# Optimization experiments

Hardware: AMD Instinct MI355X
Metric: run time of the kernel (lower is better)

## Reference

```python
import jax, jax.numpy as jnp
from jax import lax
import numpy as np
import math

EPS = 1e-5
NBINS = 17   # quantized color levels round(x*255/16) for x in [0,1)
K_MODE = 11

def _bn(x, g, b):
    # BatchNorm2d in training mode: batch statistics over (B,H,W)
    m = jnp.mean(x, axis=(0, 2, 3), keepdims=True)
    v = jnp.var(x, axis=(0, 2, 3), keepdims=True)
    return (x - m) * lax.rsqrt(v + EPS) * g[None, :, None, None] + b[None, :, None, None]

def _lrelu(x):
    return jnp.where(x >= 0, x, 0.01 * x)

def _shared_conv(x, w, b, stride, padding):
    # one KxK kernel shared depthwise across all channels, scalar bias
    C = x.shape[1]
    k = jnp.tile(w[None, None], (C, 1, 1, 1))  # (C,1,K,K)
    y = lax.conv_general_dilated(x, k, (stride, stride),
                                 [(padding, padding), (padding, padding)],
                                 dimension_numbers=('NCHW', 'OIHW', 'NCHW'),
                                 feature_group_count=C)
    return y + b[0]

def _avg_pool_same(x, k):
    # avg_pool2d(k, stride=1, padding=k//2, count_include_pad=True)
    p = k // 2
    s = lax.reduce_window(x, 0.0, lax.add, (1, 1, k, k), (1, 1, 1, 1),
                          [(0, 0), (0, 0), (p, p), (p, p)])
    return s / float(k * k)

def _mode_pool(xq):
    # xq values are exact multiples of 16/256 -> recover integer bin index,
    # then mode over 11x11 window = argmax of per-bin counts (histogram).
    # torch zero-padding corresponds to bin 0; argmax first-max tie-break ->
    # smallest value, matching torch.mode.
    q = jnp.clip(jnp.round(xq * (256.0 / 16.0)).astype(jnp.int32), 0, NBINS - 1)
    pad = K_MODE // 2
    qp = jnp.pad(q, ((0, 0), (0, 0), (pad, pad), (pad, pad)))
    onehot = (qp[:, :, None] == jnp.arange(NBINS, dtype=jnp.int32)[None, None, :, None, None]).astype(jnp.float32)
    counts = lax.reduce_window(onehot, 0.0, lax.add, (1, 1, 1, K_MODE, K_MODE), (1, 1, 1, 1, 1), 'VALID')
    mode_bin = jnp.argmax(counts, axis=2)  # (B,C,H,W)
    return mode_bin.astype(xq.dtype) * (16.0 / 256.0)

def _forward(x, p_w1, p_b1, p_dw1, p_db1, p_g1, p_be1,
             p_w2, p_b2, p_dw2, p_db2, p_g2, p_be2,
             d_w, d_b, ia_w, ia_b, ia_g, ia_be,
             ib_w, ib_b, ib_g, ib_be,
             f_g1, f_be1, f_g2, f_be2):
    xq = jnp.round(x * (255.0 / 16.0)) * (16.0 / 256.0)
    xm = _mode_pool(xq)
    B, C, H, W = xm.shape
    half = p_w1.shape[0]

    # prepare: 1x1 conv -> depthwise 1x1 (per-channel scale) -> BN -> LeakyReLU, twice
    h = jnp.einsum('bchw,oc->bohw', xm, p_w1) + p_b1[None, :, None, None]
    h = h * p_dw1[None, :, None, None] + p_db1[None, :, None, None]
    h = _lrelu(_bn(h, p_g1, p_be1))
    h = jnp.einsum('bchw,oc->bohw', h, p_w2) + p_b2[None, :, None, None]
    h = h * p_dw2[None, :, None, None] + p_db2[None, :, None, None]
    h = _lrelu(_bn(h, p_g2, p_be2))

    n = int(math.floor(math.log(min(H, W), 3)))
    score = jnp.zeros((B, 2 * half, H, W), x.dtype)
    d = h
    for _ in range(n):
        d = _shared_conv(d, d_w, d_b, 3, 1)  # stride-3 downgrade
        z = jax.image.resize(d, (B, half, H, W), method='bilinear')
        a = _lrelu(_bn(_shared_conv(z, ia_w, ia_b, 1, 2), ia_g, ia_be))
        bb = _lrelu(_bn(_shared_conv(z, ib_w, ib_b, 1, 2), ib_g, ib_be))
        score = score + jnp.concatenate([a, bb], axis=1)  # Splitter + Stack(1)

    def ft(s):
        s = _bn(s, f_g1, f_be1)
        s = jnp.where(s > 0.1, 0.1 + 0.7 * (s - 0.1), s)  # MaxLeakyReLU(0.7, 0.1)
        s = _bn(s, f_g2, f_be2)
        return 2.0 * s - _avg_pool_same(s, K_MODE)  # EmphaseLocal(11): x + (x - local mean)

    score = ft(ft(ft(score)))
    return score / n

def setup_inputs() -> dict:
    key = jax.random.key(0)
    ks = jax.random.split(key, 32)
    B, Cin, H, W, half = 8, 3, 384, 384, 32
    r = lambda i, shp, s=0.1: s * jax.random.normal(ks[i], shp, dtype=jnp.float32)
    g = lambda i, shp: 1.0 + 0.1 * jax.random.normal(ks[i], shp, dtype=jnp.float32)
    return dict(
        x=jax.random.uniform(ks[0], (B, Cin, H, W), dtype=jnp.float32),
        p_w1=r(1, (half, Cin), 0.3), p_b1=r(2, (half,)),
        p_dw1=g(3, (half,)), p_db1=r(4, (half,)),
        p_g1=g(5, (half,)), p_be1=r(6, (half,)),
        p_w2=r(7, (half, half), 0.2), p_b2=r(8, (half,)),
        p_dw2=g(9, (half,)), p_db2=r(10, (half,)),
        p_g2=g(11, (half,)), p_be2=r(12, (half,)),
        d_w=r(13, (3, 3), 0.2), d_b=r(14, (1,)),
        ia_w=r(15, (5, 5), 0.2), ia_b=r(16, (1,)),
        ia_g=g(17, (half,)), ia_be=r(18, (half,)),
        ib_w=r(19, (5, 5), 0.2), ib_b=r(20, (1,)),
        ib_g=g(21, (half,)), ib_be=r(22, (half,)),
        f_g1=g(23, (2 * half,)), f_be1=r(24, (2 * half,)),
        f_g2=g(25, (2 * half,)), f_be2=r(26, (2 * half,)),
    )

def reference(x, p_w1, p_b1, p_dw1, p_db1, p_g1, p_be1,
              p_w2, p_b2, p_dw2, p_db2, p_g2, p_be2,
              d_w, d_b, ia_w, ia_b, ia_g, ia_be,
              ib_w, ib_b, ib_g, ib_be,
              f_g1, f_be1, f_g2, f_be2):
    return _forward(x, p_w1, p_b1, p_dw1, p_db1, p_g1, p_be1,
                    p_w2, p_b2, p_dw2, p_db2, p_g2, p_be2,
                    d_w, d_b, ia_w, ia_b, ia_g, ia_be,
                    ib_w, ib_b, ib_g, ib_be,
                    f_g1, f_be1, f_g2, f_be2)
```

## Files before the change

kernel.cpp:

```cpp
#include <hip/hip_runtime.h>

#define HW 147456
#define WID 384
#define NB 8
#define NPC 1179648
#define HW4 36864

static __device__ __forceinline__ float lrelu01(float v) { return v >= 0.f ? v : 0.01f * v; }
static __device__ __forceinline__ float mlrelu(float v) { return v > 0.1f ? 0.1f + 0.7f * (v - 0.1f) : v; }

__global__ __launch_bounds__(256) void mode_kernel(const float* __restrict__ x,
                                                   float* __restrict__ xm) {
  __shared__ unsigned char qt[26 * 76];
  __shared__ unsigned int cc[16 * 5 * 76];
  const int plane = blockIdx.z;
  const int x0 = blockIdx.x * 64;
  const int y0 = blockIdx.y * 16;
  const float* xp = x + (size_t)plane * HW;

  for (int i = threadIdx.x; i < 26 * 76; i += 256) {
    int r = i / 76, ccol = i - r * 76;
    int gy = y0 + r - 5, gx = x0 + ccol - 5;
    unsigned char q = 0;
    if (ccol < 74 && gy >= 0 && gy < WID && gx >= 0 && gx < WID) {
      float v = xp[gy * WID + gx];
      int qi = (int)rintf(v * 15.9375f);
      qi = qi < 0 ? 0 : (qi > 16 ? 16 : qi);
      q = (unsigned char)qi;
    }
    qt[i] = q;
  }
  __syncthreads();

  for (int i = threadIdx.x; i < 16 * 74; i += 256) {
    int yy = i / 74, col = i - yy * 74;
    unsigned int w0 = 0, w1 = 0, w2 = 0, w3 = 0, w4 = 0;
#pragma unroll
    for (int dy = 0; dy < 11; ++dy) {
      int q = qt[(yy + dy) * 76 + col];
      unsigned int inc = 1u << ((q & 3) << 3);
      int wsel = q >> 2;
      w0 += (wsel == 0) ? inc : 0u;
      w1 += (wsel == 1) ? inc : 0u;
      w2 += (wsel == 2) ? inc : 0u;
      w3 += (wsel == 3) ? inc : 0u;
      w4 += (wsel == 4) ? inc : 0u;
    }
    cc[(yy * 5 + 0) * 76 + col] = w0;
    cc[(yy * 5 + 1) * 76 + col] = w1;
    cc[(yy * 5 + 2) * 76 + col] = w2;
    cc[(yy * 5 + 3) * 76 + col] = w3;
    cc[(yy * 5 + 4) * 76 + col] = w4;
  }
  __syncthreads();

  for (int i = threadIdx.x; i < 16 * 64; i += 256) {
    int yy = i / 64, xx = i - yy * 64;
    unsigned int s0 = 0, s1 = 0, s2 = 0, s3 = 0, s4 = 0;
#pragma unroll
    for (int dx = 0; dx < 11; ++dx) {
      int col = xx + dx;
      s0 += cc[(yy * 5 + 0) * 76 + col];
      s1 += cc[(yy * 5 + 1) * 76 + col];
      s2 += cc[(yy * 5 + 2) * 76 + col];
      s3 += cc[(yy * 5 + 3) * 76 + col];
      s4 += cc[(yy * 5 + 4) * 76 + col];
    }
    unsigned int words[5] = {s0, s1, s2, s3, s4};
    int best = 0;
    unsigned int bc = s0 & 0xffu;
#pragma unroll
    for (int bin = 1; bin < 17; ++bin) {
      unsigned int cnt = (words[bin >> 2] >> ((bin & 3) * 8)) & 0xffu;
      if (cnt > bc) { bc = cnt; best = bin; }
    }
    xm[(size_t)plane * HW + (size_t)(y0 + yy) * WID + (x0 + xx)] = best * 0.0625f;
  }
}

__global__ __launch_bounds__(256) void xm_mom(const float4* __restrict__ X,
                                              float* __restrict__ part9) {
  float s0 = 0, s1 = 0, s2 = 0, m00 = 0, m01 = 0, m02 = 0, m11 = 0, m12 = 0, m22 = 0;
  const int end = (blockIdx.x + 1) * 1152;
  for (int u = blockIdx.x * 1152 + threadIdx.x; u < end; u += 256) {
    int b = u / HW4, p4 = u - b * HW4;
    const float4* base = X + (size_t)b * 3 * HW4 + p4;
    float4 a = base[0], bb = base[HW4], c = base[2 * HW4];
    s0 += a.x + a.y + a.z + a.w;
    s1 += bb.x + bb.y + bb.z + bb.w;
    s2 += c.x + c.y + c.z + c.w;
    m00 += a.x * a.x + a.y * a.y + a.z * a.z + a.w * a.w;
    m01 += a.x * bb.x + a.y * bb.y + a.z * bb.z + a.w * bb.w;
    m02 += a.x * c.x + a.y * c.y + a.z * c.z + a.w * c.w;
    m11 += bb.x * bb.x + bb.y * bb.y + bb.z * bb.z + bb.w * bb.w;
    m12 += bb.x * c.x + bb.y * c.y + bb.z * c.z + bb.w * c.w;
    m22 += c.x * c.x + c.y * c.y + c.z * c.z + c.w * c.w;
  }
  float vals[9] = {s0, s1, s2, m00, m01, m02, m11, m12, m22};
  int lane = threadIdx.x & 63, wd = threadIdx.x >> 6;
  __shared__ float red[4][9];
#pragma unroll
  for (int j = 0; j < 9; ++j) {
    float v = vals[j];
    for (int off = 32; off; off >>= 1) v += __shfl_down(v, off);
    if (lane == 0) red[wd][j] = v;
  }
  __syncthreads();
  if (threadIdx.x < 9)
    part9[blockIdx.x * 9 + threadIdx.x] =
        red[0][threadIdx.x] + red[1][threadIdx.x] + red[2][threadIdx.x] + red[3][threadIdx.x];
}

__global__ __launch_bounds__(64) void prep1_affine(const float* __restrict__ part9,
                                                   const float* __restrict__ w1,
                                                   const float* __restrict__ b1,
                                                   const float* __restrict__ dw1,
                                                   const float* __restrict__ db1,
                                                   const float* __restrict__ g,
                                                   const float* __restrict__ be,
                                                   float* __restrict__ sc,
                                                   float* __restrict__ sh) {
  __shared__ double M[9];
  if (threadIdx.x < 9) {
    double s = 0.0;
    for (int i = 0; i < 256; ++i) s += (double)part9[i * 9 + threadIdx.x];
    M[threadIdx.x] = s;
  }
  __syncthreads();
  if (threadIdx.x < 32) {
    int o = threadIdx.x;
    double dw = dw1[o];
    double a0 = (double)w1[o * 3] * dw, a1 = (double)w1[o * 3 + 1] * dw,
           a2 = (double)w1[o * 3 + 2] * dw;
    double k = (double)b1[o] * dw + (double)db1[o];
    double N = (double)NPC;
    double lin = (a0 * M[0] + a1 * M[1] + a2 * M[2]) / N;
    double mean = lin + k;
    double e2 = (a0 * a0 * M[3] + a1 * a1 * M[6] + a2 * a2 * M[8] +
                 2.0 * (a0 * a1 * M[4] + a0 * a2 * M[5] + a1 * a2 * M[7])) / N +
                2.0 * k * lin + k * k;
    double var = e2 - mean * mean;
    float rstd = rsqrtf((float)var + 1e-5f);
    float scl = rstd * g[o];
    sc[o] = scl;
    sh[o] = be[o] - (float)mean * scl;
  }
}

__global__ __launch_bounds__(256) void prep_fused(const float* __restrict__ xm,
                                                  const float* __restrict__ w1,
                                                  const float* __restrict__ b1,
                                                  const float* __restrict__ dw1,
                                                  const float* __restrict__ db1,
                                                  const float* __restrict__ P1SC,
                                                  const float* __restrict__ P1SH,
                                                  const float* __restrict__ w2,
                                                  const float* __restrict__ b2,
                                                  const float* __restrict__ dw2,
                                                  const float* __restrict__ db2,
                                                  float* __restrict__ t2,
                                                  float* __restrict__ part) {
  __shared__ float wl[1024];
  __shared__ float c1[32][4];
  __shared__ float bias2[32];
  __shared__ float wred[8][32];
  for (int i = threadIdx.x; i < 1024; i += 256) wl[i] = w2[i] * dw2[i >> 5];
  if (threadIdx.x < 32) {
    int o = threadIdx.x;
    float dw = dw1[o], s1 = P1SC[o];
    c1[o][0] = w1[o * 3] * dw * s1;
    c1[o][1] = w1[o * 3 + 1] * dw * s1;
    c1[o][2] = w1[o * 3 + 2] * dw * s1;
    c1[o][3] = (b1[o] * dw + db1[o]) * s1 + P1SH[o];
    bias2[o] = b2[o] * dw2[o] + db2[o];
  }
  __syncthreads();
  const int p0 = blockIdx.x * 512 + threadIdx.x;
  const int b = p0 / HW, pp = p0 - b * HW;
  const float* xb = xm + (size_t)b * 3 * HW + pp;
  float h[2][32];
#pragma unroll
  for (int q = 0; q < 2; ++q) {
    float x0 = xb[q * 256], x1 = xb[HW + q * 256], x2 = xb[2 * HW + q * 256];
#pragma unroll
    for (int o = 0; o < 32; ++o) {
      float u = fmaf(x0, c1[o][0], fmaf(x1, c1[o][1], fmaf(x2, c1[o][2], c1[o][3])));
      h[q][o] = lrelu01(u);
    }
  }
  float sv[32], sq[32];
  float* ob = t2 + (size_t)b * 32 * HW + pp;
  const float4* wl4 = reinterpret_cast<const float4*>(wl);
  for (int o = 0; o < 32; ++o) {
    float acc0 = bias2[o], acc1 = bias2[o];
#pragma unroll
    for (int c4 = 0; c4 < 8; ++c4) {
      float4 w4 = wl4[o * 8 + c4];
      int c = c4 * 4;
      acc0 = fmaf(h[0][c], w4.x, acc0);     acc1 = fmaf(h[1][c], w4.x, acc1);
      acc0 = fmaf(h[0][c + 1], w4.y, acc0); acc1 = fmaf(h[1][c + 1], w4.y, acc1);
      acc0 = fmaf(h[0][c + 2], w4.z, acc0); acc1 = fmaf(h[1][c + 2], w4.z, acc1);
      acc0 = fmaf(h[0][c + 3], w4.w, acc0); acc1 = fmaf(h[1][c + 3], w4.w, acc1);
    }
    ob[(size_t)o * HW] = acc0;
    ob[(size_t)o * HW + 256] = acc1;
    sv[o] = acc0 + acc1;
    sq[o] = acc0 * acc0 + acc1 * acc1;
  }
  int lane = threadIdx.x & 63, wd = threadIdx.x >> 6;
#pragma unroll
  for (int o = 0; o < 32; ++o) {
    float a = sv[o], q = sq[o];
    for (int off = 32; off; off >>= 1) {
      a += __shfl_down(a, off);
      q += __shfl_down(q, off);
    }
    if (lane == 0) { wred[wd][o] = a; wred[wd + 4][o] = q; }
  }
  __syncthreads();
  if (threadIdx.x < 32) {
    int o = threadIdx.x;
    part[((size_t)o * 2304 + blockIdx.x) * 2] = wred[0][o] + wred[1][o] + wred[2][o] + wred[3][o];
    part[((size_t)o * 2304 + blockIdx.x) * 2 + 1] = wred[4][o] + wred[5][o] + wred[6][o] + wred[7][o];
  }
}

__global__ __launch_bounds__(64) void stats_combine(const float* __restrict__ part, int nsplit,
                                                    const float* __restrict__ g,
                                                    const float* __restrict__ be,
                                                    float* __restrict__ sc,
                                                    float* __restrict__ sh) {
  const int c = blockIdx.x;
  double s = 0.0, q = 0.0;
  for (int i = threadIdx.x; i < nsplit; i += 64) {
    s += part[((size_t)c * nsplit + i) * 2];
    q += part[((size_t)c * nsplit + i) * 2 + 1];
  }
  for (int off = 32; off; off >>= 1) {
    s += __shfl_down(s, off);
    q += __shfl_down(q, off);
  }
  if (threadIdx.x == 0) {
    double mean = s / (double)NPC;
    double var = q / (double)NPC - mean * mean;
    float rstd = rsqrtf((float)var + 1e-5f);
    float scl = rstd * g[c];
    sc[c] = scl;
    sh[c] = be[c] - (float)mean * scl;
  }
}

template <bool AFF>
__global__ __launch_bounds__(256) void dconv(const float* __restrict__ in,
                                             const float* __restrict__ sc,
                                             const float* __restrict__ sh,
                                             const float* __restrict__ w9,
                                             const float* __restrict__ db,
                                             int Sin, int Sout,
                                             float* __restrict__ out, int total) {
  int idx = blockIdx.x * 256 + threadIdx.x;
  if (idx >= total) return;
  int xx = idx % Sout;
  int t = idx / Sout;
  int yy = t % Sout;
  int pc = t / Sout;
  int c = pc & 31;
  const float* ip = in + (size_t)pc * Sin * Sin;
  float a = AFF ? sc[c] : 1.f;
  float h = AFF ? sh[c] : 0.f;
  float acc = 0.f;
#pragma unroll
  for (int ky = 0; ky < 3; ++ky) {
    int iy = 3 * yy - 1 + ky;
    if (iy < 0 || iy >= Sin) continue;
#pragma unroll
    for (int kx = 0; kx < 3; ++kx) {
      int ix = 3 * xx - 1 + kx;
      if (ix < 0 || ix >= Sin) continue;
      float v = ip[(size_t)iy * Sin + ix];
      if (AFF) { v = v * a + h; v = lrelu01(v); }
      acc = fmaf(v, w9[ky * 3 + kx], acc);
    }
  }
  out[idx] = acc + db[0];
}

static __device__ __forceinline__ int sin_of(int l) {
  return l == 0 ? 128 : l == 1 ? 43 : l == 2 ? 15 : l == 3 ? 5 : 2;
}

__device__ __forceinline__ void conv_ab(const float* zt, int row, int g,
                                        const float* wa, const float* wb,
                                        float ba0, float bb0, float* A, float* Bv) {
  float aa0 = ba0, aa1 = ba0, aa2 = ba0, aa3 = ba0;
  float eb0 = bb0, eb1 = bb0, eb2 = bb0, eb3 = bb0;
#pragma unroll
  for (int dy = 0; dy < 5; ++dy) {
    const float* zr = &zt[(row + dy) * 40 + g * 4];
    float4 zlo = *reinterpret_cast<const float4*>(zr);
    float4 zhi = *reinterpret_cast<const float4*>(zr + 4);
    float z[8] = {zlo.x, zlo.y, zlo.z, zlo.w, zhi.x, zhi.y, zhi.z, zhi.w};
#pragma unroll
    for (int dx = 0; dx < 5; ++dx) {
      float wva = wa[dy * 5 + dx], wvb = wb[dy * 5 + dx];
      aa0 = fmaf(z[dx], wva, aa0);
      aa1 = fmaf(z[dx + 1], wva, aa1);
      aa2 = fmaf(z[dx + 2], wva, aa2);
      aa3 = fmaf(z[dx + 3], wva, aa3);
      eb0 = fmaf(z[dx], wvb, eb0);
      eb1 = fmaf(z[dx + 1], wvb, eb1);
      eb2 = fmaf(z[dx + 2], wvb, eb2);
      eb3 = fmaf(z[dx + 3], wvb, eb3);
    }
  }
  A[0] = aa0; A[1] = aa1; A[2] = aa2; A[3] = aa3;
  Bv[0] = eb0; Bv[1] = eb1; Bv[2] = eb2; Bv[3] = eb3;
}

__global__ __launch_bounds__(256) void upstats2(const float* __restrict__ d1,
                                                const float* __restrict__ d2,
                                                const float* __restrict__ d3,
                                                const float* __restrict__ d4,
                                                const float* __restrict__ d5,
                                                const float* __restrict__ wA5,
                                                const float* __restrict__ wB5,
                                                const float* __restrict__ bA,
                                                const float* __restrict__ bB,
                                                float* __restrict__ partA,
                                                float* __restrict__ partB) {
  __shared__ __align__(16) float zt[2][36 * 40];
  __shared__ __align__(16) float dH[2][16 * 40];
  __shared__ int gx0[36], gx1[36], gy0[36], gy1[36];
  __shared__ float gfx[36], gfy[36], gxv[36], gyv[36];
  __shared__ float red[2][16];
  const int lvl = blockIdx.z;
  const float* dsel = lvl == 0 ? d1 : lvl == 1 ? d2 : lvl == 2 ? d3 : lvl == 3 ? d4 : d5;
  const int Sin = sin_of(lvl);
  const float scale = (float)Sin / 384.f;
  const int plane0 = blockIdx.y * 2, tile = blockIdx.x;
  const int tx = (tile % 12) * 32, ty = (tile / 12) * 32;

  if (threadIdx.x < 72) {
    int t = threadIdx.x >= 36 ? threadIdx.x - 36 : threadIdx.x;
    bool isY = threadIdx.x >= 36;
    int gp = (isY ? ty : tx) + t - 2;
    float valid = (gp >= 0 && gp < WID) ? 1.f : 0.f;
    int gpc = gp < 0 ? 0 : (gp >= WID ? WID - 1 : gp);
    float s = (gpc + 0.5f) * scale - 0.5f;
    float f0 = floorf(s);
    float fr = s - f0;
    int ii = (int)f0;
    int i1 = ii + 1 < Sin - 1 ? ii + 1 : Sin - 1;
    int i0 = ii > 0 ? ii : 0;
    if (isY) { gy0[t] = i0; gy1[t] = i1; gfy[t] = fr; gyv[t] = valid; }
    else     { gx0[t] = i0; gx1[t] = i1; gfx[t] = fr; gxv[t] = valid; }
  }
  float wa[25], wb[25];
#pragma unroll
  for (int k = 0; k < 25; ++k) { wa[k] = wA5[k]; wb[k] = wB5[k]; }
  const float ba0 = bA[0], bb0 = bB[0];
  __syncthreads();

  const int rowlo = gy0[0], nrows = gy1[35] - rowlo + 1;
  const int cnt = nrows * 36;
  for (int i = threadIdx.x; i < 2 * cnt; i += 256) {
    int p = i < cnt ? 0 : 1;
    int j = i - p * cnt;
    int r = j / 36, zx = j - r * 36;
    const float* drow = dsel + (size_t)(plane0 + p) * Sin * Sin + (size_t)(rowlo + r) * Sin;
    float v0 = drow[gx0[zx]], v1 = drow[gx1[zx]];
    dH[p][r * 40 + zx] = (v0 + gfx[zx] * (v1 - v0)) * gxv[zx];
  }
  __syncthreads();
  for (int i = threadIdx.x; i < 648; i += 256) {
    int p = i < 324 ? 0 : 1;
    int j = i - p * 324;
    int zy = j / 9, k = j - zy * 9;
    int r0 = gy0[zy] - rowlo, r1 = gy1[zy] - rowlo;
    float fy = gfy[zy], vv = gyv[zy];
    float4 a4 = *reinterpret_cast<const float4*>(&dH[p][r0 * 40 + k * 4]);
    float4 b4 = *reinterpret_cast<const float4*>(&dH[p][r1 * 40 + k * 4]);
    float4 o;
    o.x = (a4.x + fy * (b4.x - a4.x)) * vv;
    o.y = (a4.y + fy * (b4.y - a4.y)) * vv;
    o.z = (a4.z + fy * (b4.z - a4.z)) * vv;
    o.w = (a4.w + fy * (b4.w - a4.w)) * vv;
    *reinterpret_cast<float4*>(&zt[p][zy * 40 + k * 4]) = o;
  }
  __syncthreads();

  const int row = threadIdx.x >> 3, g = threadIdx.x & 7;
  const int lane = threadIdx.x & 63, wd = threadIdx.x >> 6;
#pragma unroll
  for (int p = 0; p < 2; ++p) {
    float A[4], Bv[4];
    conv_ab(zt[p], row, g, wa, wb, ba0, bb0, A, Bv);
    float sa = A[0] + A[1] + A[2] + A[3];
    float qa = A[0] * A[0] + A[1] * A[1] + A[2] * A[2] + A[3] * A[3];
    float sb = Bv[0] + Bv[1] + Bv[2] + Bv[3];
    float qb = Bv[0] * Bv[0] + Bv[1] * Bv[1] + Bv[2] * Bv[2] + Bv[3] * Bv[3];
    for (int off = 32; off; off >>= 1) {
      sa += __shfl_down(sa, off); qa += __shfl_down(qa, off);
      sb += __shfl_down(sb, off); qb += __shfl_down(qb, off);
    }
    if (lane == 0) {
      red[p][wd * 4 + 0] = sa; red[p][wd * 4 + 1] = qa;
      red[p][wd * 4 + 2] = sb; red[p][wd * 4 + 3] = qb;
    }
  }
  __syncthreads();
  if (threadIdx.x < 2) {
    int p = threadIdx.x;
    int plane = plane0 + p;
    int b = plane >> 5, c = plane & 31;
    const float* r_ = red[p];
    size_t pi = (size_t)lvl * 73728 + ((size_t)c * 1152 + (size_t)b * 144 + tile) * 2;
    partA[pi] = r_[0] + r_[4] + r_[8] + r_[12];
    partA[pi + 1] = r_[1] + r_[5] + r_[9] + r_[13];
    partB[pi] = r_[2] + r_[6] + r_[10] + r_[14];
    partB[pi + 1] = r_[3] + r_[7] + r_[11] + r_[15];
  }
}

__global__ __launch_bounds__(64) void combine_lvls(const float* __restrict__ partA,
                                                   const float* __restrict__ partB,
                                                   const float* __restrict__ ia_g,
                                                   const float* __restrict__ ia_be,
                                                   const float* __restrict__ ib_g,
                                                   const float* __restrict__ ib_be,
                                                   float* __restrict__ aff) {
  const int c = blockIdx.x, lvl = blockIdx.y, z = blockIdx.z;
  const float* part = (z ? partB : partA) + (size_t)lvl * 73728;
  const float* g = z ? ib_g : ia_g;
  const float* be = z ? ib_be : ia_be;
  double s = 0.0, q = 0.0;
  for (int i = threadIdx.x; i < 1152; i += 64) {
    s += part[((size_t)c * 1152 + i) * 2];
    q += part[((size_t)c * 1152 + i) * 2 + 1];
  }
  for (int off = 32; off; off >>= 1) {
    s += __shfl_down(s, off);
    q += __shfl_down(q, off);
  }
  if (threadIdx.x == 0) {
    double mean = s / (double)NPC;
    double var = q / (double)NPC - mean * mean;
    float rstd = rsqrtf((float)var + 1e-5f);
    float scl = rstd * g[c];
    aff[((z * 5 + lvl) * 2 + 0) * 32 + c] = scl;
    aff[((z * 5 + lvl) * 2 + 1) * 32 + c] = be[c] - (float)mean * scl;
  }
}

__global__ __launch_bounds__(256) void apply_all(const float* __restrict__ d1,
                                                 const float* __restrict__ d2,
                                                 const float* __restrict__ d3,
                                                 const float* __restrict__ d4,
                                                 const float* __restrict__ d5,
                                                 const float* __restrict__ wA5,
                                                 const float* __restrict__ wB5,
                                                 const float* __restrict__ bA,
                                                 const float* __restrict__ bB,
                                                 const float* __restrict__ aff,
                                                 float* __restrict__ outp,
                                                 float* __restrict__ partF) {
  __shared__ __align__(16) float zt[36 * 40];
  __shared__ __align__(16) float dH[16 * 40];
  __shared__ int gx0[5][36], gx1[5][36], gy0[5][36], gy1[5][36];
  __shared__ float gfx[5][36], gfy[5][36], gxv[5][36], gyv[5][36];
  __shared__ float red[16];
  const int plane = blockIdx.y, tile = blockIdx.x;
  const int tx = (tile % 12) * 32, ty = (tile / 12) * 32;
  const int b = plane >> 5, c = plane & 31;
  float wa[25], wb[25];
#pragma unroll
  for (int k = 0; k < 25; ++k) { wa[k] = wA5[k]; wb[k] = wB5[k]; }
  const float ba0 = bA[0], bb0 = bB[0];
  const int row = threadIdx.x >> 3, g = threadIdx.x & 7;

  for (int i = threadIdx.x; i < 360; i += 256) {
    int l = i / 72, j = i - l * 72;
    int t = j >= 36 ? j - 36 : j;
    bool isY = j >= 36;
    int Sin = sin_of(l);
    float scale = (float)Sin / 384.f;
    int gp = (isY ? ty : tx) + t - 2;
    float valid = (gp >= 0 && gp < WID) ? 1.f : 0.f;
    int gpc = gp < 0 ? 0 : (gp >= WID ? WID - 1 : gp);
    float s = (gpc + 0.5f) * scale - 0.5f;
    float f0 = floorf(s);
    float fr = s - f0;
    int ii = (int)f0;
    int i1 = ii + 1 < Sin - 1 ? ii + 1 : Sin - 1;
    int i0 = ii > 0 ? ii : 0;
    if (isY) { gy0[l][t] = i0; gy1[l][t] = i1; gfy[l][t] = fr; gyv[l][t] = valid; }
    else     { gx0[l][t] = i0; gx1[l][t] = i1; gfx[l][t] = fr; gxv[l][t] = valid; }
  }
  __syncthreads();

  float acA[4] = {0.f, 0.f, 0.f, 0.f}, acB[4] = {0.f, 0.f, 0.f, 0.f};
  for (int l = 0; l < 5; ++l) {
    const float* dsel = l == 0 ? d1 : l == 1 ? d2 : l == 2 ? d3 : l == 3 ? d4 : d5;
    const int Sin = sin_of(l);
    const float* dp = dsel + (size_t)plane * Sin * Sin;
    const int rowlo = gy0[l][0], nrows = gy1[l][35] - rowlo + 1;
    for (int i = threadIdx.x; i < nrows * 36; i += 256) {
      int r = i / 36, zx = i - r * 36;
      const float* drow = dp + (size_t)(rowlo + r) * Sin;
      float v0 = drow[gx0[l][zx]], v1 = drow[gx1[l][zx]];
      dH[r * 40 + zx] = (v0 + gfx[l][zx] * (v1 - v0)) * gxv[l][zx];
    }
    __syncthreads();
    for (int i = threadIdx.x; i < 324; i += 256) {
      int zy = i / 9, k = i - zy * 9;
      int r0 = gy0[l][zy] - rowlo, r1 = gy1[l][zy] - rowlo;
      float fy = gfy[l][zy], vv = gyv[l][zy];
      float4 a4 = *reinterpret_cast<const float4*>(&dH[r0 * 40 + k * 4]);
      float4 b4 = *reinterpret_cast<const float4*>(&dH[r1 * 40 + k * 4]);
      float4 o;
      o.x = (a4.x + fy * (b4.x - a4.x)) * vv;
      o.y = (a4.y + fy * (b4.y - a4.y)) * vv;
      o.z = (a4.z + fy * (b4.z - a4.z)) * vv;
      o.w = (a4.w + fy * (b4.w - a4.w)) * vv;
      *reinterpret_cast<float4*>(&zt[zy * 40 + k * 4]) = o;
    }
    __syncthreads();
    float A[4], Bv[4];
    conv_ab(zt, row, g, wa, wb, ba0, bb0, A, Bv);
    float as = aff[(l * 2 + 0) * 32 + c], ah = aff[(l * 2 + 1) * 32 + c];
    float bs = aff[((5 + l) * 2 + 0) * 32 + c], bh = aff[((5 + l) * 2 + 1) * 32 + c];
#pragma unroll
    for (int j = 0; j < 4; ++j) {
      acA[j] += lrelu01(fmaf(A[j], as, ah));
      acB[j] += lrelu01(fmaf(Bv[j], bs, bh));
    }
  }
  float4 xa = {acA[0], acA[1], acA[2], acA[3]};
  float4 xb = {acB[0], acB[1], acB[2], acB[3]};
  size_t po = (size_t)(b * 64 + c) * HW + (size_t)(ty + row) * WID + tx + g * 4;
  *reinterpret_cast<float4*>(outp + po) = xa;
  *reinterpret_cast<float4*>(outp + po + (size_t)32 * HW) = xb;

  float sa = xa.x + xa.y + xa.z + xa.w;
  float qa = xa.x * xa.x + xa.y * xa.y + xa.z * xa.z + xa.w * xa.w;
  float sb = xb.x + xb.y + xb.z + xb.w;
  float qb = xb.x * xb.x + xb.y * xb.y + xb.z * xb.z + xb.w * xb.w;
  int lane = threadIdx.x & 63, wd = threadIdx.x >> 6;
  for (int off = 32; off; off >>= 1) {
    sa += __shfl_down(sa, off); qa += __shfl_down(qa, off);
    sb += __shfl_down(sb, off); qb += __shfl_down(qb, off);
  }
  __syncthreads();
  if (lane == 0) {
    red[wd * 4 + 0] = sa; red[wd * 4 + 1] = qa;
    red[wd * 4 + 2] = sb; red[wd * 4 + 3] = qb;
  }
  __syncthreads();
  if (threadIdx.x == 0) {
    size_t piA = ((size_t)c * 1152 + (size_t)b * 144 + tile) * 2;
    size_t piB = ((size_t)(c + 32) * 1152 + (size_t)b * 144 + tile) * 2;
    partF[piA] = red[0] + red[4] + red[8] + red[12];
    partF[piA + 1] = red[1] + red[5] + red[9] + red[13];
    partF[piB] = red[2] + red[6] + red[10] + red[14];
    partF[piB + 1] = red[3] + red[7] + red[11] + red[15];
  }
}

__global__ __launch_bounds__(256) void stats_mlrelu(const float4* __restrict__ X,
                                                    const float* __restrict__ sc1,
                                                    const float* __restrict__ sh1,
                                                    float* __restrict__ part) {
  int c = blockIdx.x >> 6, s = blockIdx.x & 63;
  float a1 = sc1[c], b1 = sh1[c];
  float sum = 0.f, sq = 0.f;
  int b = s >> 3;
  const float4* Xp = X + (size_t)(b * 64 + c) * HW4 + (s & 7) * 4608 + threadIdx.x;
#pragma unroll 6
  for (int it = 0; it < 18; ++it) {
    float4 v = Xp[it * 256];
    float u;
    u = mlrelu(fmaf(v.x, a1, b1)); sum += u; sq += u * u;
    u = mlrelu(fmaf(v.y, a1, b1)); sum += u; sq += u * u;
    u = mlrelu(fmaf(v.z, a1, b1)); sum += u; sq += u * u;
    u = mlrelu(fmaf(v.w, a1, b1)); sum += u; sq += u * u;
  }
  int lane = threadIdx.x & 63, wd = threadIdx.x >> 6;
  for (int off = 32; off; off >>= 1) {
    sum += __shfl_down(sum, off);
    sq += __shfl_down(sq, off);
  }
  __shared__ float red[8];
  if (lane == 0) { red[wd * 2] = sum; red[wd * 2 + 1] = sq; }
  __syncthreads();
  if (threadIdx.x == 0) {
    part[((size_t)c * 64 + s) * 2] = red[0] + red[2] + red[4] + red[6];
    part[((size_t)c * 64 + s) * 2 + 1] = red[1] + red[3] + red[5] + red[7];
  }
}

__global__ __launch_bounds__(256) void ft_fused(const float* __restrict__ src,
                                                const float* __restrict__ F1SC,
                                                const float* __restrict__ F1SH,
                                                const float* __restrict__ F2SC,
                                                const float* __restrict__ F2SH,
                                                float* __restrict__ dst, float fscale,
                                                float* __restrict__ part) {
  __shared__ float sl[74 * 81];
  __shared__ __align__(16) float Hl[74 * 64];
  __shared__ float red[8];
  const int tile = blockIdx.x;
  const int plane = blockIdx.y;
  const int b = plane >> 6, c = plane & 63;
  const int tx = (tile % 6) * 64, ty = (tile / 6) * 64;
  const float a1 = F1SC[c], b1 = F1SH[c], a2 = F2SC[c], b2 = F2SH[c];
  const float* sp = src + (size_t)plane * HW;

  for (int i = threadIdx.x; i < 74 * 20; i += 256) {
    int r = i / 20, k = i - r * 20;
    int gy = ty + r - 5, gx = tx + k * 4 - 8;
    float4 sv = {0.f, 0.f, 0.f, 0.f};
    if (gy >= 0 && gy < WID && gx >= 0 && gx < WID) {
      float4 v = *reinterpret_cast<const float4*>(sp + (size_t)gy * WID + gx);
      sv.x = fmaf(mlrelu(fmaf(v.x, a1, b1)), a2, b2);
      sv.y = fmaf(mlrelu(fmaf(v.y, a1, b1)), a2, b2);
      sv.z = fmaf(mlrelu(fmaf(v.z, a1, b1)), a2, b2);
      sv.w = fmaf(mlrelu(fmaf(v.w, a1, b1)), a2, b2);
    }
    int base = r * 81 + k * 4;
    sl[base] = sv.x; sl[base + 1] = sv.y; sl[base + 2] = sv.z; sl[base + 3] = sv.w;
  }
  __syncthreads();

  for (int i = threadIdx.x; i < 74 * 16; i += 256) {
    int r = i >> 4, g = i & 15;
    const float* s0 = &sl[r * 81 + g * 4 + 3];
    float v[14];
#pragma unroll
    for (int j = 0; j < 14; ++j) v[j] = s0[j];
    float h0 = v[0] + v[1] + v[2] + v[3] + v[4] + v[5] + v[6] + v[7] + v[8] + v[9] + v[10];
    float h1 = h0 - v[0] + v[11];
    float h2 = h1 - v[1] + v[12];
    float h3 = h2 - v[2] + v[13];
    float4 hh = {h0, h1, h2, h3};
    *reinterpret_cast<float4*>(&Hl[r * 64 + g * 4]) = hh;
  }
  __syncthreads();

  const int g = threadIdx.x & 15, ly = threadIdx.x >> 4;
  const int y0 = ly * 4;
  const float4* H4 = reinterpret_cast<const float4*>(Hl);
  float4 acc = H4[y0 * 16 + g];
#pragma unroll
  for (int dy = 1; dy < 11; ++dy) {
    float4 t = H4[(y0 + dy) * 16 + g];
    acc.x += t.x; acc.y += t.y; acc.z += t.z; acc.w += t.w;
  }
  float sum = 0.f, sq = 0.f;
  float* dpo = dst + (size_t)plane * HW;
#pragma unroll
  for (int ry = 0; ry < 4; ++ry) {
    int y = y0 + ry;
    if (ry) {
      float4 ta = H4[(y + 10) * 16 + g];
      float4 tb = H4[(y - 1) * 16 + g];
      acc.x += ta.x - tb.x; acc.y += ta.y - tb.y;
      acc.z += ta.z - tb.z; acc.w += ta.w - tb.w;
    }
    const float* cp = &sl[(y + 5) * 81 + g * 4 + 8];
    float4 o;
    o.x = (2.f * cp[0] - acc.x * (1.f / 121.f)) * fscale;
    o.y = (2.f * cp[1] - acc.y * (1.f / 121.f)) * fscale;
    o.z = (2.f * cp[2] - acc.z * (1.f / 121.f)) * fscale;
    o.w = (2.f * cp[3] - acc.w * (1.f / 121.f)) * fscale;
    *reinterpret_cast<float4*>(dpo + (size_t)(ty + y) * WID + tx + g * 4) = o;
    sum += o.x + o.y + o.z + o.w;
    sq += o.x * o.x + o.y * o.y + o.z * o.z + o.w * o.w;
  }
  if (part) {
    int lane = threadIdx.x & 63, wd = threadIdx.x >> 6;
    for (int off = 32; off; off >>= 1) {
      sum += __shfl_down(sum, off);
      sq += __shfl_down(sq, off);
    }
    if (lane == 0) { red[wd * 2] = sum; red[wd * 2 + 1] = sq; }
    __syncthreads();
    if (threadIdx.x == 0) {
      size_t pi = ((size_t)c * 288 + (size_t)b * 36 + tile) * 2;
      part[pi] = red[0] + red[2] + red[4] + red[6];
      part[pi + 1] = red[1] + red[3] + red[5] + red[7];
    }
  }
}

extern "C" void kernel_launch(void* const* d_in, const int* in_sizes, int n_in,
                              void* d_out, int out_size, void* d_ws, size_t ws_size,
                              hipStream_t stream) {
  const float* x     = (const float*)d_in[0];
  const float* p_w1  = (const float*)d_in[1];
  const float* p_b1  = (const float*)d_in[2];
  const float* p_dw1 = (const float*)d_in[3];
  const float* p_db1 = (const float*)d_in[4];
  const float* p_g1  = (const float*)d_in[5];
  const float* p_be1 = (const float*)d_in[6];
  const float* p_w2  = (const float*)d_in[7];
  const float* p_b2  = (const float*)d_in[8];
  const float* p_dw2 = (const float*)d_in[9];
  const float* p_db2 = (const float*)d_in[10];
  const float* p_g2  = (const float*)d_in[11];
  const float* p_be2 = (const float*)d_in[12];
  const float* d_w   = (const float*)d_in[13];
  const float* d_b   = (const float*)d_in[14];
  const float* ia_w  = (const float*)d_in[15];
  const float* ia_b  = (const float*)d_in[16];
  const float* ia_g  = (const float*)d_in[17];
  const float* ia_be = (const float*)d_in[18];
  const float* ib_w  = (const float*)d_in[19];
  const float* ib_b  = (const float*)d_in[20];
  const float* ib_g  = (const float*)d_in[21];
  const float* ib_be = (const float*)d_in[22];
  const float* f_g1  = (const float*)d_in[23];
  const float* f_be1 = (const float*)d_in[24];
  const float* f_g2  = (const float*)d_in[25];
  const float* f_be2 = (const float*)d_in[26];
  float* out = (float*)d_out;
  float* ws = (float*)d_ws;

  const size_t SLOT = 37748736ull;
  float* B0 = ws;
  float* B1 = ws + 2 * SLOT;
  float* t2 = B0;
  float* partA = B0 + SLOT;
  float* partB = partA + 368640;
  float* partP = partB + 368640;
  float* part9 = partP + 147456;
  float* aff   = part9 + 2304;
  float* xm  = B1;
  float* dd1 = xm + 3538944;
  float* dd2 = dd1 + 4194304;
  float* dd3 = dd2 + 473344;
  float* dd4 = dd3 + 57600;
  float* dd5 = dd4 + 6400;
  float* partF = ws + 4 * SLOT;
  float* partS = partF + 147456;
  float* st    = partS + 8192;

  float* P1SC = st,       *P1SH = st + 32;
  float* P2SC = st + 64,  *P2SH = st + 96;
  float* F1SC = st + 128, *F1SH = st + 192;
  float* F2SC = st + 256, *F2SH = st + 320;

  mode_kernel<<<dim3(6, 24, 24), 256, 0, stream>>>(x, xm);
  xm_mom<<<256, 256, 0, stream>>>((const float4*)xm, part9);
  prep1_affine<<<1, 64, 0, stream>>>(part9, p_w1, p_b1, p_dw1, p_db1, p_g1, p_be1, P1SC, P1SH);
  prep_fused<<<2304, 256, 0, stream>>>(xm, p_w1, p_b1, p_dw1, p_db1, P1SC, P1SH,
                                       p_w2, p_b2, p_dw2, p_db2, t2, partP);
  stats_combine<<<32, 64, 0, stream>>>(partP, 2304, p_g2, p_be2, P2SC, P2SH);

  dconv<true><<<16384, 256, 0, stream>>>(t2, P2SC, P2SH, d_w, d_b, 384, 128, dd1,
                                         8 * 32 * 128 * 128);
  dconv<false><<<(8 * 32 * 43 * 43 + 255) / 256, 256, 0, stream>>>(
      dd1, nullptr, nullptr, d_w, d_b, 128, 43, dd2, 8 * 32 * 43 * 43);
  dconv<false><<<(8 * 32 * 15 * 15 + 255) / 256, 256, 0, stream>>>(
      dd2, nullptr, nullptr, d_w, d_b, 43, 15, dd3, 8 * 32 * 15 * 15);
  dconv<false><<<(8 * 32 * 5 * 5 + 255) / 256, 256, 0, stream>>>(
      dd3, nullptr, nullptr, d_w, d_b, 15, 5, dd4, 8 * 32 * 5 * 5);
  dconv<false><<<(8 * 32 * 2 * 2 + 255) / 256, 256, 0, stream>>>(
      dd4, nullptr, nullptr, d_w, d_b, 5, 2, dd5, 8 * 32 * 2 * 2);

  upstats2<<<dim3(144, 128, 5), 256, 0, stream>>>(dd1, dd2, dd3, dd4, dd5,
                                                  ia_w, ib_w, ia_b, ib_b, partA, partB);
  combine_lvls<<<dim3(32, 5, 2), 64, 0, stream>>>(partA, partB, ia_g, ia_be, ib_g, ib_be, aff);
  apply_all<<<dim3(144, 256), 256, 0, stream>>>(dd1, dd2, dd3, dd4, dd5,
                                                ia_w, ib_w, ia_b, ib_b, aff, out, partF);

  const float* cur = out;
  float* dsts[3] = {B0, B1, out};
  for (int k = 0; k < 3; ++k) {
    stats_combine<<<64, 64, 0, stream>>>(partF, (k == 0) ? 1152 : 288, f_g1, f_be1, F1SC, F1SH);
    stats_mlrelu<<<64 * 64, 256, 0, stream>>>((const float4*)cur, F1SC, F1SH, partS);
    stats_combine<<<64, 64, 0, stream>>>(partS, 64, f_g2, f_be2, F2SC, F2SH);
    ft_fused<<<dim3(36, 512), 256, 0, stream>>>(cur, F1SC, F1SH, F2SC, F2SH, dsts[k],
                                                (k == 2) ? 0.2f : 1.0f,
                                                (k < 2) ? partF : nullptr);
    cur = dsts[k];
  }
}
```

Baseline: 2.097 ms.

## Split pyramid upsample-conv into per-wave row strips with wave-local LDS fences

Measured after the change: 2.260 ms. +7.8%, slower.

```diff
diff --git a/kernel.cpp b/kernel.cpp
--- a/kernel.cpp
+++ b/kernel.cpp
@@ -8,6 +8,9 @@
 
 static __device__ __forceinline__ float lrelu01(float v) { return v >= 0.f ? v : 0.01f * v; }
 static __device__ __forceinline__ float mlrelu(float v) { return v > 0.1f ? 0.1f + 0.7f * (v - 0.1f) : v; }
+
+#define WFENCE() do { asm volatile("s_waitcnt lgkmcnt(0)" ::: "memory"); \
+                      __builtin_amdgcn_sched_barrier(0); } while (0)
 
 __global__ __launch_bounds__(256) void mode_kernel(const float* __restrict__ x,
                                                    float* __restrict__ xm) {
@@ -317,166 +320,36 @@
   Bv[0] = eb0; Bv[1] = eb1; Bv[2] = eb2; Bv[3] = eb3;
 }
 
-__global__ __launch_bounds__(256) void upstats2(const float* __restrict__ d1,
-                                                const float* __restrict__ d2,
-                                                const float* __restrict__ d3,
-                                                const float* __restrict__ d4,
-                                                const float* __restrict__ d5,
-                                                const float* __restrict__ wA5,
-                                                const float* __restrict__ wB5,
-                                                const float* __restrict__ bA,
-                                                const float* __restrict__ bB,
-                                                float* __restrict__ partA,
-                                                float* __restrict__ partB) {
-  __shared__ __align__(16) float zt[2][36 * 40];
-  __shared__ __align__(16) float dH[2][16 * 40];
-  __shared__ int gx0[36], gx1[36], gy0[36], gy1[36];
-  __shared__ float gfx[36], gfy[36], gxv[36], gyv[36];
-  __shared__ float red[2][16];
-  const int lvl = blockIdx.z;
-  const float* dsel = lvl == 0 ? d1 : lvl == 1 ? d2 : lvl == 2 ? d3 : lvl == 3 ? d4 : d5;
-  const int Sin = sin_of(lvl);
-  const float scale = (float)Sin / 384.f;
-  const int plane0 = blockIdx.y * 2, tile = blockIdx.x;
-  const int tx = (tile % 12) * 32, ty = (tile / 12) * 32;
-
-  if (threadIdx.x < 72) {
-    int t = threadIdx.x >= 36 ? threadIdx.x - 36 : threadIdx.x;
-    bool isY = threadIdx.x >= 36;
-    int gp = (isY ? ty : tx) + t - 2;
-    float valid = (gp >= 0 && gp < WID) ? 1.f : 0.f;
-    int gpc = gp < 0 ? 0 : (gp >= WID ? WID - 1 : gp);
-    float s = (gpc + 0.5f) * scale - 0.5f;
-    float f0 = floorf(s);
-    float fr = s - f0;
-    int ii = (int)f0;
-    int i1 = ii + 1 < Sin - 1 ? ii + 1 : Sin - 1;
-    int i0 = ii > 0 ? ii : 0;
-    if (isY) { gy0[t] = i0; gy1[t] = i1; gfy[t] = fr; gyv[t] = valid; }
-    else     { gx0[t] = i0; gx1[t] = i1; gfx[t] = fr; gxv[t] = valid; }
-  }
-  float wa[25], wb[25];
-#pragma unroll
-  for (int k = 0; k < 25; ++k) { wa[k] = wA5[k]; wb[k] = wB5[k]; }
-  const float ba0 = bA[0], bb0 = bB[0];
-  __syncthreads();
-
-  const int rowlo = gy0[0], nrows = gy1[35] - rowlo + 1;
-  const int cnt = nrows * 36;
-  for (int i = threadIdx.x; i < 2 * cnt; i += 256) {
-    int p = i < cnt ? 0 : 1;
-    int j = i - p * cnt;
-    int r = j / 36, zx = j - r * 36;
-    const float* drow = dsel + (size_t)(plane0 + p) * Sin * Sin + (size_t)(rowlo + r) * Sin;
-    float v0 = drow[gx0[zx]], v1 = drow[gx1[zx]];
-    dH[p][r * 40 + zx] = (v0 + gfx[zx] * (v1 - v0)) * gxv[zx];
-  }
-  __syncthreads();
-  for (int i = threadIdx.x; i < 648; i += 256) {
-    int p = i < 324 ? 0 : 1;
-    int j = i - p * 324;
-    int zy = j / 9, k = j - zy * 9;
-    int r0 = gy0[zy] - rowlo, r1 = gy1[zy] - rowlo;
-    float fy = gfy[zy], vv = gyv[zy];
-    float4 a4 = *reinterpret_cast<const float4*>(&dH[p][r0 * 40 + k * 4]);
-    float4 b4 = *reinterpret_cast<const float4*>(&dH[p][r1 * 40 + k * 4]);
-    float4 o;
-    o.x = (a4.x + fy * (b4.x - a4.x)) * vv;
-    o.y = (a4.y + fy * (b4.y - a4.y)) * vv;
-    o.z = (a4.z + fy * (b4.z - a4.z)) * vv;
-    o.w = (a4.w + fy * (b4.w - a4.w)) * vv;
-    *reinterpret_cast<float4*>(&zt[p][zy * 40 + k * 4]) = o;
-  }
-  __syncthreads();
-
-  const int row = threadIdx.x >> 3, g = threadIdx.x & 7;
-  const int lane = threadIdx.x & 63, wd = threadIdx.x >> 6;
-#pragma unroll
-  for (int p = 0; p < 2; ++p) {
-    float A[4], Bv[4];
-    conv_ab(zt[p], row, g, wa, wb, ba0, bb0, A, Bv);
-    float sa = A[0] + A[1] + A[2] + A[3];
-    float qa = A[0] * A[0] + A[1] * A[1] + A[2] * A[2] + A[3] * A[3];
-    float sb = Bv[0] + Bv[1] + Bv[2] + Bv[3];
-    float qb = Bv[0] * Bv[0] + Bv[1] * Bv[1] + Bv[2] * Bv[2] + Bv[3] * Bv[3];
-    for (int off = 32; off; off >>= 1) {
-      sa += __shfl_down(sa, off); qa += __shfl_down(qa, off);
-      sb += __shfl_down(sb, off); qb += __shfl_down(qb, off);
-    }
-    if (lane == 0) {
-      red[p][wd * 4 + 0] = sa; red[p][wd * 4 + 1] = qa;
-      red[p][wd * 4 + 2] = sb; red[p][wd * 4 + 3] = qb;
-    }
-  }
-  __syncthreads();
-  if (threadIdx.x < 2) {
-    int p = threadIdx.x;
-    int plane = plane0 + p;
-    int b = plane >> 5, c = plane & 31;
-    const float* r_ = red[p];
-    size_t pi = (size_t)lvl * 73728 + ((size_t)c * 1152 + (size_t)b * 144 + tile) * 2;
-    partA[pi] = r_[0] + r_[4] + r_[8] + r_[12];
-    partA[pi + 1] = r_[1] + r_[5] + r_[9] + r_[13];
-    partB[pi] = r_[2] + r_[6] + r_[10] + r_[14];
-    partB[pi + 1] = r_[3] + r_[7] + r_[11] + r_[15];
-  }
-}
-
-__global__ __launch_bounds__(64) void combine_lvls(const float* __restrict__ partA,
-                                                   const float* __restrict__ partB,
-                                                   const float* __restrict__ ia_g,
-                                                   const float* __restrict__ ia_be,
-                                                   const float* __restrict__ ib_g,
-                                                   const float* __restrict__ ib_be,
-                                                   float* __restrict__ aff) {
-  const int c = blockIdx.x, lvl = blockIdx.y, z = blockIdx.z;
-  const float* part = (z ? partB : partA) + (size_t)lvl * 73728;
-  const float* g = z ? ib_g : ia_g;
-  const float* be = z ? ib_be : ia_be;
-  double s = 0.0, q = 0.0;
-  for (int i = threadIdx.x; i < 1152; i += 64) {
-    s += part[((size_t)c * 1152 + i) * 2];
-    q += part[((size_t)c * 1152 + i) * 2 + 1];
-  }
-  for (int off = 32; off; off >>= 1) {
-    s += __shfl_down(s, off);
-    q += __shfl_down(q, off);
-  }
-  if (threadIdx.x == 0) {
-    double mean = s / (double)NPC;
-    double var = q / (double)NPC - mean * mean;
-    float rstd = rsqrtf((float)var + 1e-5f);
-    float scl = rstd * g[c];
-    aff[((z * 5 + lvl) * 2 + 0) * 32 + c] = scl;
-    aff[((z * 5 + lvl) * 2 + 1) * 32 + c] = be[c] - (float)mean * scl;
-  }
-}
-
-__global__ __launch_bounds__(256) void apply_all(const float* __restrict__ d1,
-                                                 const float* __restrict__ d2,
-                                                 const float* __restrict__ d3,
-                                                 const float* __restrict__ d4,
-                                                 const float* __restrict__ d5,
-                                                 const float* __restrict__ wA5,
-                                                 const float* __restrict__ wB5,
-                                                 const float* __restrict__ bA,
-                                                 const float* __restrict__ bB,
-                                                 const float* __restrict__ aff,
-                                                 float* __restrict__ outp,
-                                                 float* __restrict__ partF) {
-  __shared__ __align__(16) float zt[36 * 40];
-  __shared__ __align__(16) float dH[16 * 40];
+template <bool APPLY>
+__global__ __launch_bounds__(256) void pyr_wave(
+    const float* __restrict__ d1, const float* __restrict__ d2,
+    const float* __restrict__ d3, const float* __restrict__ d4,
+    const float* __restrict__ d5,
+    const float* __restrict__ wA5, const float* __restrict__ wB5,
+    const float* __restrict__ bA, const float* __restrict__ bB,
+    const float* __restrict__ aff, float* __restrict__ outp,
+    float* __restrict__ partA, float* __restrict__ partB,
+    float* __restrict__ partF) {
+  __shared__ __align__(16) float ztS[4][12 * 40];
+  __shared__ __align__(16) float dHS[4][8 * 40];
   __shared__ int gx0[5][36], gx1[5][36], gy0[5][36], gy1[5][36];
   __shared__ float gfx[5][36], gfy[5][36], gxv[5][36], gyv[5][36];
-  __shared__ float red[16];
+  __shared__ float red[80];
+
   const int plane = blockIdx.y, tile = blockIdx.x;
   const int tx = (tile % 12) * 32, ty = (tile / 12) * 32;
   const int b = plane >> 5, c = plane & 31;
+  const int wv = threadIdx.x >> 6;
+  const int lane = threadIdx.x & 63;
+  float* ztw = ztS[wv];
+  float* dHw = dHS[wv];
+  const int zlo = wv * 8;
+
   float wa[25], wb[25];
 #pragma unroll
   for (int k = 0; k < 25; ++k) { wa[k] = wA5[k]; wb[k] = wB5[k]; }
   const float ba0 = bA[0], bb0 = bB[0];
-  const int row = threadIdx.x >> 3, g = threadIdx.x & 7;
+  const int row = lane >> 3, g = lane & 7;
 
   for (int i = threadIdx.x; i < 360; i += 256) {
     int l = i / 72, j = i - l * 72;
@@ -503,66 +376,128 @@
     const float* dsel = l == 0 ? d1 : l == 1 ? d2 : l == 2 ? d3 : l == 3 ? d4 : d5;
     const int Sin = sin_of(l);
     const float* dp = dsel + (size_t)plane * Sin * Sin;
-    const int rowlo = gy0[l][0], nrows = gy1[l][35] - rowlo + 1;
-    for (int i = threadIdx.x; i < nrows * 36; i += 256) {
+    const int rowlo = gy0[l][zlo];
+    const int nr = gy1[l][zlo + 11] - rowlo + 1;
+    for (int i = lane; i < nr * 36; i += 64) {
       int r = i / 36, zx = i - r * 36;
       const float* drow = dp + (size_t)(rowlo + r) * Sin;
       float v0 = drow[gx0[l][zx]], v1 = drow[gx1[l][zx]];
-      dH[r * 40 + zx] = (v0 + gfx[l][zx] * (v1 - v0)) * gxv[l][zx];
-    }
-    __syncthreads();
-    for (int i = threadIdx.x; i < 324; i += 256) {
-      int zy = i / 9, k = i - zy * 9;
+      dHw[r * 40 + zx] = (v0 + gfx[l][zx] * (v1 - v0)) * gxv[l][zx];
+    }
+    WFENCE();
+    for (int i = lane; i < 108; i += 64) {
+      int j = i / 9, k = i - j * 9;
+      int zy = zlo + j;
       int r0 = gy0[l][zy] - rowlo, r1 = gy1[l][zy] - rowlo;
       float fy = gfy[l][zy], vv = gyv[l][zy];
-      float4 a4 = *reinterpret_cast<const float4*>(&dH[r0 * 40 + k * 4]);
-      float4 b4 = *reinterpret_cast<const float4*>(&dH[r1 * 40 + k * 4]);
+      float4 a4 = *reinterpret_cast<const float4*>(&dHw[r0 * 40 + k * 4]);
+      float4 b4 = *reinterpret_cast<const float4*>(&dHw[r1 * 40 + k * 4]);
       float4 o;
       o.x = (a4.x + fy * (b4.x - a4.x)) * vv;
       o.y = (a4.y + fy * (b4.y - a4.y)) * vv;
       o.z = (a4.z + fy * (b4.z - a4.z)) * vv;
       o.w = (a4.w + fy * (b4.w - a4.w)) * vv;
-      *reinterpret_cast<float4*>(&zt[zy * 40 + k * 4]) = o;
+      *reinterpret_cast<float4*>(&ztw[j * 40 + k * 4]) = o;
+    }
+    WFENCE();
+    float A[4], Bv[4];
+    conv_ab(ztw, row, g, wa, wb, ba0, bb0, A, Bv);
+    if (APPLY) {
+      float as = aff[(l * 2 + 0) * 32 + c], ah = aff[(l * 2 + 1) * 32 + c];
+      float bs = aff[((5 + l) * 2 + 0) * 32 + c], bh = aff[((5 + l) * 2 + 1) * 32 + c];
+#pragma unroll
+      for (int j = 0; j < 4; ++j) {
+        acA[j] += lrelu01(fmaf(A[j], as, ah));
+        acB[j] += lrelu01(fmaf(Bv[j], bs, bh));
+      }
+    } else {
+      float sa = A[0] + A[1] + A[2] + A[3];
+      float qa = A[0] * A[0] + A[1] * A[1] + A[2] * A[2] + A[3] * A[3];
+      float sb = Bv[0] + Bv[1] + Bv[2] + Bv[3];
+      float qb = Bv[0] * Bv[0] + Bv[1] * Bv[1] + Bv[2] * Bv[2] + Bv[3] * Bv[3];
+      for (int off = 32; off; off >>= 1) {
+        sa += __shfl_down(sa, off); qa += __shfl_down(qa, off);
+        sb += __shfl_down(sb, off); qb += __shfl_down(qb, off);
+      }
+      if (lane == 0) {
+        red[l * 16 + wv * 4 + 0] = sa;
+        red[l * 16 + wv * 4 + 1] = qa;
+        red[l * 16 + wv * 4 + 2] = sb;
+        red[l * 16 + wv * 4 + 3] = qb;
+      }
+    }
+  }
+
+  if (APPLY) {
+    float4 xa = {acA[0], acA[1], acA[2], acA[3]};
+    float4 xb = {acB[0], acB[1], acB[2], acB[3]};
+    size_t po = (size_t)(b * 64 + c) * HW + (size_t)(ty + zlo + row) * WID + tx + g * 4;
+    *reinterpret_cast<float4*>(outp + po) = xa;
+    *reinterpret_cast<float4*>(outp + po + (size_t)32 * HW) = xb;
+    float sa = xa.x + xa.y + xa.z + xa.w;
+    float qa = xa.x * xa.x + xa.y * xa.y + xa.z * xa.z + xa.w * xa.w;
+    float sb = xb.x + xb.y + xb.z + xb.w;
+    float qb = xb.x * xb.x + xb.y * xb.y + xb.z * xb.z + xb.w * xb.w;
+    for (int off = 32; off; off >>= 1) {
+      sa += __shfl_down(sa, off); qa += __shfl_down(qa, off);
+      sb += __shfl_down(sb, off); qb += __shfl_down(qb, off);
+    }
+    if (lane == 0) {
+      red[wv * 4 + 0] = sa; red[wv * 4 + 1] = qa;
+      red[wv * 4 + 2] = sb; red[wv * 4 + 3] = qb;
     }
     __syncthreads();
-    float A[4], Bv[4];
-    conv_ab(zt, row, g, wa, wb, ba0, bb0, A, Bv);
-    float as = aff[(l * 2 + 0) * 32 + c], ah = aff[(l * 2 + 1) * 32 + c];
-    float bs = aff[((5 + l) * 2 + 0) * 32 + c], bh = aff[((5 + l) * 2 + 1) * 32 + c];
-#pragma unroll
-    for (int j = 0; j < 4; ++j) {
-      acA[j] += lrelu01(fmaf(A[j], as, ah));
-      acB[j] += lrelu01(fmaf(Bv[j], bs, bh));
-    }
-  }
-  float4 xa = {acA[0], acA[1], acA[2], acA[3]};
-  float4 xb = {acB[0], acB[1], acB[2], acB[3]};
-  size_t po = (size_t)(b * 64 + c) * HW + (size_t)(ty + row) * WID + tx + g * 4;
-  *reinterpret_cast<float4*>(outp + po) = xa;
-  *reinterpret_cast<float4*>(outp + po + (size_t)32 * HW) = xb;
-
-  float sa = xa.x + xa.y + xa.z + xa.w;
-  float qa = xa.x * xa.x + xa.y * xa.y + xa.z * xa.z + xa.w * xa.w;
-  float sb = xb.x + xb.y + xb.z + xb.w;
-  float qb = xb.x * xb.x + xb.y * xb.y + xb.z * xb.z + xb.w * xb.w;
-  int lane = threadIdx.x & 63, wd = threadIdx.x >> 6;
+    if (threadIdx.x == 0) {
+      size_t piA = ((size_t)c * 1152 + (size_t)b * 144 + tile) * 2;
+      size_t piB = ((size_t)(c + 32) * 1152 + (size_t)b * 144 + tile) * 2;
+      partF[piA] = red[0] + red[4] + red[8] + red[12];
+      partF[piA + 1] = red[1] + red[5] + red[9] + red[13];
+      partF[piB] = red[2] + red[6] + red[10] + red[14];
+      partF[piB + 1] = red[3] + red[7] + red[11] + red[15];
+    }
+  } else {
+    __syncthreads();
+    if (threadIdx.x < 5) {
+      int l = threadIdx.x;
+      const float* rl_ = &red[l * 16];
+      float SA = rl_[0] + rl_[4] + rl_[8] + rl_[12];
+      float QA = rl_[1] + rl_[5] + rl_[9] + rl_[13];
+      float SB = rl_[2] + rl_[6] + rl_[10] + rl_[14];
+      float QB = rl_[3] + rl_[7] + rl_[11] + rl_[15];
+      size_t pi = (size_t)l * 73728 + ((size_t)c * 1152 + (size_t)b * 144 + tile) * 2;
+      partA[pi] = SA; partA[pi + 1] = QA;
+      partB[pi] = SB; partB[pi + 1] = QB;
+    }
+  }
+}
+
+__global__ __launch_bounds__(64) void combine_lvls(const float* __restrict__ partA,
+                                                   const float* __restrict__ partB,
+                                                   const float* __restrict__ ia_g,
+                                                   const float* __restrict__ ia_be,
+                                                   const float* __restrict__ ib_g,
+                                                   const float* __restrict__ ib_be,
+                                                   float* __restrict__ aff) {
+  const int c = blockIdx.x, lvl = blockIdx.y, z = blockIdx.z;
+  const float* part = (z ? partB : partA) + (size_t)lvl * 73728;
+  const float* g = z ? ib_g : ia_g;
+  const float* be = z ? ib_be : ia_be;
+  double s = 0.0, q = 0.0;
+  for (int i = threadIdx.x; i < 1152; i += 64) {
+    s += part[((size_t)c * 1152 + i) * 2];
+    q += part[((size_t)c * 1152 + i) * 2 + 1];
+  }
   for (int off = 32; off; off >>= 1) {
-    sa += __shfl_down(sa, off); qa += __shfl_down(qa, off);
-    sb += __shfl_down(sb, off); qb += __shfl_down(qb, off);
-  }
-  __syncthreads();
-  if (lane == 0) {
-    red[wd * 4 + 0] = sa; red[wd * 4 + 1] = qa;
-    red[wd * 4 + 2] = sb; red[wd * 4 + 3] = qb;
-  }
-  __syncthreads();
+    s += __shfl_down(s, off);
+    q += __shfl_down(q, off);
+  }
   if (threadIdx.x == 0) {
-    size_t piA = ((size_t)c * 1152 + (size_t)b * 144 + tile) * 2;
-    size_t piB = ((size_t)(c + 32) * 1152 + (size_t)b * 144 + tile) * 2;
-    partF[piA] = red[0] + red[4] + red[8] + red[12];
-    partF[piA + 1] = red[1] + red[5] + red[9] + red[13];
-    partF[piB] = red[2] + red[6] + red[10] + red[14];
-    partF[piB + 1] = red[3] + red[7] + red[11] + red[15];
+    double mean = s / (double)NPC;
+    double var = q / (double)NPC - mean * mean;
+    float rstd = rsqrtf((float)var + 1e-5f);
+    float scl = rstd * g[c];
+    aff[((z * 5 + lvl) * 2 + 0) * 32 + c] = scl;
+    aff[((z * 5 + lvl) * 2 + 1) * 32 + c] = be[c] - (float)mean * scl;
   }
 }
 
@@ -767,11 +702,13 @@
   dconv<false><<<(8 * 32 * 2 * 2 + 255) / 256, 256, 0, stream>>>(
       dd4, nullptr, nullptr, d_w, d_b, 5, 2, dd5, 8 * 32 * 2 * 2);
 
-  upstats2<<<dim3(144, 128, 5), 256, 0, stream>>>(dd1, dd2, dd3, dd4, dd5,
-                                                  ia_w, ib_w, ia_b, ib_b, partA, partB);
+  pyr_wave<false><<<dim3(144, 256), 256, 0, stream>>>(
+      dd1, dd2, dd3, dd4, dd5, ia_w, ib_w, ia_b, ib_b,
+      nullptr, nullptr, partA, partB, nullptr);
   combine_lvls<<<dim3(32, 5, 2), 64, 0, stream>>>(partA, partB, ia_g, ia_be, ib_g, ib_be, aff);
-  apply_all<<<dim3(144, 256), 256, 0, stream>>>(dd1, dd2, dd3, dd4, dd5,
-                                                ia_w, ib_w, ia_b, ib_b, aff, out, partF);
+  pyr_wave<true><<<dim3(144, 256), 256, 0, stream>>>(
+      dd1, dd2, dd3, dd4, dd5, ia_w, ib_w, ia_b, ib_b,
+      aff, out, nullptr, nullptr, partF);
 
   const float* cur = out;
   float* dsts[3] = {B0, B1, out};
```
